# Optimization experiments

Hardware: AMD Instinct MI355X
Metric: run time of the kernel (lower is better)

## Reference

```python
import jax, jax.numpy as jnp
import numpy as np

B, N, C, H = 4, 2048, 1024, 16
D = C // H  # head_dim


def setup_inputs() -> dict:
    key = jax.random.key(0)
    ks = jax.random.split(key, 9)
    s = 1.0 / np.sqrt(C)
    return {
        "x": jax.random.normal(ks[0], (B, N, C), dtype=jnp.float32),
        "Wq": jax.random.uniform(ks[1], (C, C), jnp.float32, -s, s),
        "bq": jax.random.uniform(ks[2], (C,), jnp.float32, -s, s),
        "Wk": jax.random.uniform(ks[3], (C, C), jnp.float32, -s, s),
        "bk": jax.random.uniform(ks[4], (C,), jnp.float32, -s, s),
        "Wv": jax.random.uniform(ks[5], (C, C), jnp.float32, -s, s),
        "bv": jax.random.uniform(ks[6], (C,), jnp.float32, -s, s),
        "Wo": jax.random.uniform(ks[7], (C, C), jnp.float32, -s, s),
        "bo": jax.random.uniform(ks[8], (C,), jnp.float32, -s, s),
    }


def reference(x, Wq, bq, Wk, bk, Wv, bv, Wo, bo):
    # QKV projections -> [B, H, N, D]
    def proj(W, b):
        y = jnp.einsum('bnc,cd->bnd', x, W) + b
        return y.reshape(B, N, H, D).transpose(0, 2, 1, 3)

    q = proj(Wq, bq)
    k = proj(Wk, bk)
    v = proj(Wv, bv)

    scale = 1.0 / np.sqrt(D).astype(np.float32)
    scores = jnp.einsum('bhnd,bhmd->bhnm', q, k) * scale  # [B,H,N,N]
    probs = jax.nn.softmax(scores, axis=-1)
    out = jnp.einsum('bhnm,bhmd->bhnd', probs, v)  # [B,H,N,D]
    out = out.transpose(0, 2, 1, 3).reshape(B, N, C)
    return jnp.einsum('bnc,cd->bnd', out, Wo) + bo
```

## Files before the change

### kernel.cpp

```cpp
#include <hip/hip_runtime.h>
#include <hip/hip_bf16.h>
#include <stdint.h>


#define DEV __device__ __forceinline__

typedef unsigned short u16;
typedef __attribute__((ext_vector_type(8))) _Float16 f16x8;
typedef __attribute__((ext_vector_type(2))) _Float16 f16x2;
typedef __attribute__((ext_vector_type(4))) float f32x4;

DEV u16 f2h(float f) {
    _Float16 h = (_Float16)f;
    return __builtin_bit_cast(u16, h);
}

DEV unsigned int pk2h(float a, float b) {
    return __builtin_bit_cast(unsigned int, __builtin_amdgcn_cvt_pkrtz(a, b));
}

#define GLD16(gp, lp)                                                         \
    __builtin_amdgcn_global_load_lds(                                         \
        (__attribute__((address_space(1))) void*)(gp),                        \
        (__attribute__((address_space(3))) void*)(lp), 16, 0, 0)

DEV f32x4 mfma16(f16x8 a, f16x8 b, f32x4 c) {
    return __builtin_amdgcn_mfma_f32_16x16x32_f16(a, b, c, 0, 0, 0);
}

__global__ void cast_fuse(const float* __restrict__ x,
                          const float* __restrict__ Wq, const float* __restrict__ Wk,
                          const float* __restrict__ Wv, const float* __restrict__ Wo,
                          u16* __restrict__ xb, u16* __restrict__ Wt4) {
    __shared__ float lds[64 * 68];
    int bid = blockIdx.x, tid = threadIdx.x;
    if (bid < 4096) {
        size_t base = (size_t)bid * 2048 + (size_t)tid * 8;
        float4 v0 = *(const float4*)(x + base);
        float4 v1 = *(const float4*)(x + base + 4);
        union { u16 u[8]; uint4 v; } p;
        p.u[0] = f2h(v0.x); p.u[1] = f2h(v0.y); p.u[2] = f2h(v0.z); p.u[3] = f2h(v0.w);
        p.u[4] = f2h(v1.x); p.u[5] = f2h(v1.y); p.u[6] = f2h(v1.z); p.u[7] = f2h(v1.w);
        *(uint4*)(xb + base) = p.v;
        return;
    }
    bid -= 4096;
    int wsel = bid >> 8, t = bid & 255;
    int k0 = (t >> 4) * 64, n0 = (t & 15) * 64;
    const float* W = wsel == 0 ? Wq : wsel == 1 ? Wk : wsel == 2 ? Wv : Wo;
    u16* Wt = Wt4 + (size_t)wsel * 1048576;
#pragma unroll
    for (int i = 0; i < 4; i++) {
        int slot = tid * 4 + i * 1024;
        int rr = slot >> 6, cc = slot & 63;
        float4 v = *(const float4*)(W + (size_t)(k0 + rr) * 1024 + n0 + cc);
        *(float4*)(&lds[rr * 68 + cc]) = v;
    }
    __syncthreads();
    int n = tid >> 2, kc = (tid & 3) * 16;
    union { u16 u[16]; uint4 v[2]; } p;
#pragma unroll
    for (int j = 0; j < 16; j++) p.u[j] = f2h(lds[(kc + j) * 68 + n]);
    u16* dst = Wt + (size_t)(n0 + n) * 1024 + k0 + kc;
    *(uint4*)(dst) = p.v[0];
    *(uint4*)(dst + 8) = p.v[1];
}

DEV void gemm_core(const u16* __restrict__ A, const u16* __restrict__ Wt,
                   int m0, int n0, f32x4 (&acc)[4][4]) {
    __shared__ u16 Alds[2][128 * 32];
    __shared__ u16 Blds[2][128 * 32];
    const int tid = threadIdx.x, lane = tid & 63;
    const int w = tid >> 6, g = lane >> 4, r16 = lane & 15;
    const int wm = (w >> 1) * 64, wn = (w & 1) * 64;
#pragma unroll
    for (int i = 0; i < 4; i++)
#pragma unroll
        for (int j = 0; j < 4; j++) acc[i][j] = f32x4{0.f, 0.f, 0.f, 0.f};

    auto stage = [&](int buf, int kt) {
        int k0 = kt * 64;
#pragma unroll
        for (int i = 0; i < 2; i++) {
            int slot = i * 4096 + tid * 16;
            int rr = slot >> 6, cc = slot & 63;
            GLD16((const char*)A + (size_t)(m0 + rr) * 2048 + k0 + cc,
                  (char*)Alds[buf] + slot);
            GLD16((const char*)Wt + (size_t)(n0 + rr) * 2048 + k0 + cc,
                  (char*)Blds[buf] + slot);
        }
    };
    stage(0, 0);
    __syncthreads();

    for (int kt = 0; kt < 32; ++kt) {
        int cur = kt & 1;
        if (kt < 31) stage(cur ^ 1, kt + 1);
        f16x8 af[4], bf[4];
#pragma unroll
        for (int i = 0; i < 4; i++) {
            af[i] = *(const f16x8*)((const char*)Alds[cur] + (wm + i * 16 + r16) * 64 + g * 16);
            bf[i] = *(const f16x8*)((const char*)Blds[cur] + (wn + i * 16 + r16) * 64 + g * 16);
        }
#pragma unroll
        for (int i = 0; i < 4; i++)
#pragma unroll
            for (int j = 0; j < 4; j++) acc[i][j] = mfma16(af[i], bf[j], acc[i][j]);
        __syncthreads();
    }
}

__global__ __launch_bounds__(256, 2) void gemm_qkv(
    const u16* __restrict__ xb, const u16* __restrict__ Wt4,
    const float* __restrict__ bq, const float* __restrict__ bk,
    const float* __restrict__ bv,
    u16* __restrict__ Qo, u16* __restrict__ Ko, u16* __restrict__ Vo) {
    int m0 = blockIdx.x * 128, n0 = blockIdx.y * 128, z = blockIdx.z;
    const u16* Wt = Wt4 + (size_t)z * 1048576;
    const float* bias = z == 0 ? bq : z == 1 ? bk : bv;
    u16* Out = z == 0 ? Qo : z == 1 ? Ko : Vo;
    const float sc = (z == 0) ? 0.125f * 1.44269504f : 1.0f;
    f32x4 acc[4][4];
    gemm_core(xb, Wt, m0, n0, acc);
    const int lane = threadIdx.x & 63, w = threadIdx.x >> 6;
    const int g = lane >> 4, r16 = lane & 15;
    const int wm = (w >> 1) * 64, wn = (w & 1) * 64;
#pragma unroll
    for (int j = 0; j < 4; j++) {
        int c = n0 + wn + j * 16 + r16;
        float bb = bias[c];
        int h = c >> 6, d = c & 63;
#pragma unroll
        for (int i = 0; i < 4; i++) {
#pragma unroll
            for (int rr = 0; rr < 4; rr++) {
                int m = m0 + wm + i * 16 + g * 4 + rr;
                int b = m >> 11, n = m & 2047;
                Out[(((size_t)(b * 16 + h)) * 2048 + n) * 64 + d] =
                    f2h((acc[i][j][rr] + bb) * sc);
            }
        }
    }
}

__global__ __launch_bounds__(256, 2) void gemm_out(
    const u16* __restrict__ AO, const u16* __restrict__ Wt,
    const float* __restrict__ bo, float* __restrict__ Out) {
    int m0 = blockIdx.x * 128, n0 = blockIdx.y * 128;
    f32x4 acc[4][4];
    gemm_core(AO, Wt, m0, n0, acc);
    const int lane = threadIdx.x & 63, w = threadIdx.x >> 6;
    const int g = lane >> 4, r16 = lane & 15;
    const int wm = (w >> 1) * 64, wn = (w & 1) * 64;
#pragma unroll
    for (int j = 0; j < 4; j++) {
        int c = n0 + wn + j * 16 + r16;
        float bb = bo[c];
#pragma unroll
        for (int i = 0; i < 4; i++) {
#pragma unroll
            for (int rr = 0; rr < 4; rr++) {
                int m = m0 + wm + i * 16 + g * 4 + rr;
                Out[(size_t)m * 1024 + c] = acc[i][j][rr] + bb;
            }
        }
    }
}

__global__ void transpose_v(const u16* __restrict__ V, u16* __restrict__ VT) {
    __shared__ u16 lds[64 * 66];
    int bh = blockIdx.x >> 5, n0 = (blockIdx.x & 31) * 64;
    const u16* Vb = V + (size_t)bh * 2048 * 64;
    u16* VTb = VT + (size_t)bh * 64 * 2048;
    int tid = threadIdx.x;
#pragma unroll
    for (int i = 0; i < 8; i++) {
        int p = tid + i * 256;
        int rr = p >> 5, c2 = (p & 31) * 2;
        unsigned int val = *(const unsigned int*)(Vb + (size_t)(n0 + rr) * 64 + c2);
        *(unsigned int*)(&lds[rr * 66 + c2]) = val;
    }
    __syncthreads();
#pragma unroll
    for (int i = 0; i < 2; i++) {
        int s = tid * 8 + i * 2048;
        int d = s >> 6, ns = s & 63;
        union { u16 u[8]; uint4 v; } p;
#pragma unroll
        for (int j = 0; j < 8; j++) p.u[j] = lds[(ns + j) * 66 + d];
        *(uint4*)(VTb + (size_t)d * 2048 + n0 + ns) = p.v;
    }
}

__global__ __launch_bounds__(256, 2) void attn_k(
    const u16* __restrict__ Q, const u16* __restrict__ K,
    const u16* __restrict__ VT, u16* __restrict__ AO) {
    __shared__ char Klds[2][16384];
    __shared__ char Vlds[2][16384];
    __shared__ char Plds[4][4096];
    const int bh = blockIdx.x, q0 = blockIdx.y * 128;
    const int tid = threadIdx.x, lane = tid & 63, w = tid >> 6;
    const int g = lane >> 4, r16 = lane & 15;
    const char* Qb = (const char*)(Q + (size_t)bh * 2048 * 64);
    const char* Kb = (const char*)(K + (size_t)bh * 2048 * 64);
    const char* VTb = (const char*)(VT + (size_t)bh * 64 * 2048);
    char* Pw = Plds[w];
    const f32x4 ZZ = {0.f, 0.f, 0.f, 0.f};

    f16x8 qf[2][2];
#pragma unroll
    for (int qg = 0; qg < 2; qg++)
#pragma unroll
        for (int ks = 0; ks < 2; ks++)
            qf[qg][ks] = *(const f16x8*)(Qb + (size_t)(q0 + w * 32 + qg * 16 + r16) * 128 +
                                         ks * 64 + g * 16);
    f16x8 onesf;
#pragma unroll
    for (int j = 0; j < 8; j++) onesf[j] = (_Float16)1.0f;

    f32x4 oacc[2][4], lacc[2];
#pragma unroll
    for (int qg = 0; qg < 2; qg++) {
#pragma unroll
        for (int dg = 0; dg < 4; dg++) oacc[qg][dg] = ZZ;
        lacc[qg] = ZZ;
    }

    auto stage = [&](int buf, int t) {
#pragma unroll
        for (int i = 0; i < 4; i++) {
            int slot = i * 4096 + tid * 16;
            {
                int rr = slot >> 7, cc = slot & 127;
                GLD16(Kb + (size_t)(t * 128 + rr) * 128 + (cc ^ ((rr & 7) << 4)),
                      Klds[buf] + slot);
            }
            {
                int rr = slot >> 8, cc = slot & 255;
                GLD16(VTb + (size_t)rr * 4096 + t * 256 + (cc ^ ((rr & 7) << 4)),
                      Vlds[buf] + slot);
            }
        }
    };
    stage(0, 0);
    __syncthreads();

    for (int t = 0; t < 16; ++t) {
        const int cur = t & 1;
        if (t < 15) stage(cur ^ 1, t + 1);
        const char* Kl = Klds[cur];
        const char* Vl = Vlds[cur];

        f32x4 sacc[8][2];
        __builtin_amdgcn_s_setprio(1);
#pragma unroll
        for (int kg = 0; kg < 8; kg++) {
            int row = kg * 16 + r16, sw = (row & 7) << 4;
            f16x8 kf0 = *(const f16x8*)(Kl + row * 128 + ((g * 16) ^ sw));
            f16x8 kf1 = *(const f16x8*)(Kl + row * 128 + ((64 + g * 16) ^ sw));
#pragma unroll
            for (int qg = 0; qg < 2; qg++) {
                sacc[kg][qg] = mfma16(kf0, qf[qg][0], ZZ);
                sacc[kg][qg] = mfma16(kf1, qf[qg][1], sacc[kg][qg]);
            }
        }
        __builtin_amdgcn_s_setprio(0);

#pragma unroll
        for (int h = 0; h < 2; h++) {
#pragma unroll
            for (int qg = 0; qg < 2; qg++) {
#pragma unroll
                for (int kg2 = 0; kg2 < 4; kg2++) {
                    int kg = h * 4 + kg2;
                    uint2 pk;
                    pk.x = pk2h(exp2f(sacc[kg][qg][0]), exp2f(sacc[kg][qg][1]));
                    pk.y = pk2h(exp2f(sacc[kg][qg][2]), exp2f(sacc[kg][qg][3]));
                    *(uint2*)(Pw + (qg * 16 + r16) * 128 +
                              ((kg2 * 32 + g * 8) ^ ((r16 & 7) << 4))) = pk;
                }
            }
            __builtin_amdgcn_s_setprio(1);
#pragma unroll
            for (int ks2 = 0; ks2 < 2; ks2++) {
                f16x8 pf[2], vf[4];
#pragma unroll
                for (int qg = 0; qg < 2; qg++) {
                    int row = qg * 16 + r16;
                    pf[qg] = *(const f16x8*)(Pw + row * 128 +
                                             ((ks2 * 64 + g * 16) ^ ((r16 & 7) << 4)));
                }
#pragma unroll
                for (int dg = 0; dg < 4; dg++) {
                    int row = dg * 16 + r16;
                    vf[dg] = *(const f16x8*)(Vl + row * 256 +
                                             ((h * 128 + ks2 * 64 + g * 16) ^ ((row & 7) << 4)));
                }
#pragma unroll
                for (int qg = 0; qg < 2; qg++) {
#pragma unroll
                    for (int dg = 0; dg < 4; dg++)
                        oacc[qg][dg] = mfma16(pf[qg], vf[dg], oacc[qg][dg]);
                    lacc[qg] = mfma16(pf[qg], onesf, lacc[qg]);
                }
            }
            __builtin_amdgcn_s_setprio(0);
        }
        __syncthreads();
    }

    const int b = bh >> 4, h = bh & 15;
#pragma unroll
    for (int qg = 0; qg < 2; qg++) {
        float li[4];
#pragma unroll
        for (int rr = 0; rr < 4; rr++) li[rr] = 1.0f / lacc[qg][rr];
#pragma unroll
        for (int dg = 0; dg < 4; dg++) {
            int d = dg * 16 + r16;
#pragma unroll
            for (int rr = 0; rr < 4; rr++) {
                int nrow = q0 + w * 32 + qg * 16 + g * 4 + rr;
                AO[((size_t)(b * 2048 + nrow)) * 1024 + h * 64 + d] =
                    f2h(oacc[qg][dg][rr] * li[rr]);
            }
        }
    }
}

extern "C" void kernel_launch(void* const* d_in, const int* in_sizes, int n_in,
                              void* d_out, int out_size, void* d_ws, size_t ws_size,
                              hipStream_t stream) {
    const float* x = (const float*)d_in[0];
    const float* Wq = (const float*)d_in[1];
    const float* bq = (const float*)d_in[2];
    const float* Wk = (const float*)d_in[3];
    const float* bk = (const float*)d_in[4];
    const float* Wv = (const float*)d_in[5];
    const float* bv = (const float*)d_in[6];
    const float* Wo = (const float*)d_in[7];
    const float* bo = (const float*)d_in[8];

    char* ws = (char*)d_ws;
    u16* xb  = (u16*)(ws);
    u16* Wt  = (u16*)(ws + (16ull << 20));
    u16* Qb  = (u16*)(ws + (24ull << 20));
    u16* Kb  = (u16*)(ws + (40ull << 20));
    u16* Vb  = (u16*)(ws + (56ull << 20));
    u16* VTb = (u16*)(ws + (72ull << 20));
    u16* AO  = (u16*)(ws + (88ull << 20));

    cast_fuse<<<dim3(5120), dim3(256), 0, stream>>>(x, Wq, Wk, Wv, Wo, xb, Wt);
    gemm_qkv<<<dim3(64, 8, 3), dim3(256), 0, stream>>>(xb, Wt, bq, bk, bv, Qb, Kb, Vb);
    transpose_v<<<dim3(2048), dim3(256), 0, stream>>>(Vb, VTb);
    attn_k<<<dim3(64, 16), dim3(256), 0, stream>>>(Qb, Kb, VTb, AO);
    gemm_out<<<dim3(64, 8), dim3(256), 0, stream>>>(AO, Wt + 3ull * 1048576, bo,
                                                    (float*)d_out);
}
```

Baseline: 311.3 us.

## Enlarge GEMM tiles to 256x256 with swizzled LDS and interleaved pipeline

Replaces the 128x128, 4-wave GEMM core with a 256x256, 8-wave core for the QKV and output projections. It uses K-steps of 128, an XOR swizzle on the LDS layout to cut bank conflicts, and staged half-tile loads interleaved with MFMA phases under s_setprio and explicit barriers. The intent is to raise arithmetic intensity and hide global-to-LDS latency behind compute. The cost is far fewer blocks (384 and 128, versus a CU count of 256 on MI355X), so the wave fills the GPU poorly. The design also carries heavy LDS usage (128KB per block), register pressure, and many barriers.

Measured after the change: 340.4 us. 1.09x slower.

```diff
diff --git a/kernel.cpp b/kernel.cpp
--- a/kernel.cpp
+++ b/kernel.cpp
@@ -7,7 +7,6 @@
 
 typedef unsigned short u16;
 typedef __attribute__((ext_vector_type(8))) _Float16 f16x8;
-typedef __attribute__((ext_vector_type(2))) _Float16 f16x2;
 typedef __attribute__((ext_vector_type(4))) float f32x4;
 
 DEV u16 f2h(float f) {
@@ -27,6 +26,8 @@
 DEV f32x4 mfma16(f16x8 a, f16x8 b, f32x4 c) {
     return __builtin_amdgcn_mfma_f32_16x16x32_f16(a, b, c, 0, 0, 0);
 }
+
+DEV int swz(int lin) { return lin ^ (((lin >> 9) & 1) << 5); }
 
 __global__ void cast_fuse(const float* __restrict__ x,
                           const float* __restrict__ Wq, const float* __restrict__ Wk,
@@ -66,102 +67,152 @@
     *(uint4*)(dst + 8) = p.v[1];
 }
 
-DEV void gemm_core(const u16* __restrict__ A, const u16* __restrict__ Wt,
-                   int m0, int n0, f32x4 (&acc)[4][4]) {
-    __shared__ u16 Alds[2][128 * 32];
-    __shared__ u16 Blds[2][128 * 32];
+DEV void gemm_core256(const u16* __restrict__ A, const u16* __restrict__ Bw,
+                      int m0, int n0, f32x4 (&acc)[8][4]) {
+    __shared__ u16 Al[2][2][128 * 64];
+    __shared__ u16 Bl[2][2][128 * 64];
     const int tid = threadIdx.x, lane = tid & 63;
     const int w = tid >> 6, g = lane >> 4, r16 = lane & 15;
-    const int wm = (w >> 1) * 64, wn = (w & 1) * 64;
-#pragma unroll
-    for (int i = 0; i < 4; i++)
-#pragma unroll
-        for (int j = 0; j < 4; j++) acc[i][j] = f32x4{0.f, 0.f, 0.f, 0.f};
-
-    auto stage = [&](int buf, int kt) {
-        int k0 = kt * 64;
-#pragma unroll
-        for (int i = 0; i < 2; i++) {
-            int slot = i * 4096 + tid * 16;
-            int rr = slot >> 6, cc = slot & 63;
-            GLD16((const char*)A + (size_t)(m0 + rr) * 2048 + k0 + cc,
-                  (char*)Alds[buf] + slot);
-            GLD16((const char*)Wt + (size_t)(n0 + rr) * 2048 + k0 + cc,
-                  (char*)Blds[buf] + slot);
+    const int wm_id = w >> 2, wnh = (w & 3) >> 1, wnl = w & 1;
+
+#pragma unroll
+    for (int mi = 0; mi < 8; mi++)
+#pragma unroll
+        for (int nj = 0; nj < 4; nj++) acc[mi][nj] = f32x4{0.f, 0.f, 0.f, 0.f};
+
+    auto stage = [&](int buf, int h, int T) {
+        const bool isB = (h & 2) != 0;
+        const int half = h & 1;
+        char* dst = (char*)(isB ? Bl[buf][half] : Al[buf][half]);
+        const char* src = (const char*)(isB ? Bw : A);
+        const int r0 = (isB ? n0 : m0) + half * 128;
+#pragma unroll
+        for (int j = 0; j < 2; ++j) {
+            int slot = j * 8192 + tid * 16;
+            int lin = swz(slot);
+            int row = lin >> 7, c2 = lin & 127;
+            GLD16(src + (size_t)(r0 + row) * 2048 + T * 128 + c2, dst + slot);
         }
     };
-    stage(0, 0);
-    __syncthreads();
-
-    for (int kt = 0; kt < 32; ++kt) {
-        int cur = kt & 1;
-        if (kt < 31) stage(cur ^ 1, kt + 1);
-        f16x8 af[4], bf[4];
-#pragma unroll
-        for (int i = 0; i < 4; i++) {
-            af[i] = *(const f16x8*)((const char*)Alds[cur] + (wm + i * 16 + r16) * 64 + g * 16);
-            bf[i] = *(const f16x8*)((const char*)Blds[cur] + (wn + i * 16 + r16) * 64 + g * 16);
-        }
-#pragma unroll
-        for (int i = 0; i < 4; i++)
-#pragma unroll
-            for (int j = 0; j < 4; j++) acc[i][j] = mfma16(af[i], bf[j], acc[i][j]);
-        __syncthreads();
-    }
-}
-
-__global__ __launch_bounds__(256, 2) void gemm_qkv(
+    auto lda = [&](f16x8 (&af)[4][2], int mq, const char* Ah) {
+#pragma unroll
+        for (int mi = 0; mi < 4; ++mi)
+#pragma unroll
+            for (int ks = 0; ks < 2; ++ks) {
+                int lin = (mq * 64 + mi * 16 + r16) * 128 + ks * 64 + g * 16;
+                af[mi][ks] = *(const f16x8*)(Ah + swz(lin));
+            }
+    };
+    auto ldb = [&](f16x8 (&bf)[2][2], int nq, const char* Bh) {
+#pragma unroll
+        for (int nj = 0; nj < 2; ++nj)
+#pragma unroll
+            for (int ks = 0; ks < 2; ++ks) {
+                int lin = (wnl * 64 + nq * 32 + nj * 16 + r16) * 128 + ks * 64 + g * 16;
+                bf[nj][ks] = *(const f16x8*)(Bh + swz(lin));
+            }
+    };
+    auto mm = [&](int mq, int nq, f16x8 (&af)[4][2], f16x8 (&bf)[2][2]) {
+        __builtin_amdgcn_s_setprio(1);
+#pragma unroll
+        for (int mi = 0; mi < 4; ++mi)
+#pragma unroll
+            for (int nj = 0; nj < 2; ++nj) {
+                f32x4 c = acc[mq * 4 + mi][nq * 2 + nj];
+                c = mfma16(af[mi][0], bf[nj][0], c);
+                c = mfma16(af[mi][1], bf[nj][1], c);
+                acc[mq * 4 + mi][nq * 2 + nj] = c;
+            }
+        __builtin_amdgcn_s_setprio(0);
+    };
+
+#pragma unroll
+    for (int h = 0; h < 4; ++h) stage(0, h, 0);
+    stage(1, 0, 1);
+    asm volatile("s_waitcnt vmcnt(2)" ::: "memory");
+    __builtin_amdgcn_s_barrier();
+
+    for (int T = 0; T < 16; ++T) {
+        const int buf = T & 1;
+        const char* Ah = (const char*)Al[buf][wm_id];
+        const char* Bh = (const char*)Bl[buf][wnh];
+        f16x8 af[4][2], bfA[2][2], bfB[2][2];
+        lda(af, 0, Ah);
+        ldb(bfA, 0, Bh);
+        if (T + 1 < 16) stage(buf ^ 1, 1, T + 1);
+        __builtin_amdgcn_s_barrier();
+        mm(0, 0, af, bfA);
+        __builtin_amdgcn_s_barrier();
+        ldb(bfB, 1, Bh);
+        if (T + 1 < 16) stage(buf ^ 1, 2, T + 1);
+        __builtin_amdgcn_s_barrier();
+        mm(0, 1, af, bfB);
+        __builtin_amdgcn_s_barrier();
+        lda(af, 1, Ah);
+        if (T + 1 < 16) stage(buf ^ 1, 3, T + 1);
+        __builtin_amdgcn_s_barrier();
+        mm(1, 0, af, bfA);
+        __builtin_amdgcn_s_barrier();
+        if (T + 2 < 16) stage(buf, 0, T + 2);
+        __builtin_amdgcn_s_barrier();
+        mm(1, 1, af, bfB);
+        asm volatile("s_waitcnt vmcnt(2)" ::: "memory");
+        __builtin_amdgcn_s_barrier();
+    }
+}
+
+__global__ __launch_bounds__(512, 2) void gemm_qkv(
     const u16* __restrict__ xb, const u16* __restrict__ Wt4,
     const float* __restrict__ bq, const float* __restrict__ bk,
     const float* __restrict__ bv,
     u16* __restrict__ Qo, u16* __restrict__ Ko, u16* __restrict__ Vo) {
-    int m0 = blockIdx.x * 128, n0 = blockIdx.y * 128, z = blockIdx.z;
+    int m0 = blockIdx.x * 256, n0 = blockIdx.y * 256, z = blockIdx.z;
     const u16* Wt = Wt4 + (size_t)z * 1048576;
     const float* bias = z == 0 ? bq : z == 1 ? bk : bv;
     u16* Out = z == 0 ? Qo : z == 1 ? Ko : Vo;
     const float sc = (z == 0) ? 0.125f * 1.44269504f : 1.0f;
-    f32x4 acc[4][4];
-    gemm_core(xb, Wt, m0, n0, acc);
+    f32x4 acc[8][4];
+    gemm_core256(xb, Wt, m0, n0, acc);
     const int lane = threadIdx.x & 63, w = threadIdx.x >> 6;
     const int g = lane >> 4, r16 = lane & 15;
-    const int wm = (w >> 1) * 64, wn = (w & 1) * 64;
-#pragma unroll
-    for (int j = 0; j < 4; j++) {
-        int c = n0 + wn + j * 16 + r16;
+    const int wm0 = m0 + (w >> 2) * 128, wn0 = n0 + (w & 3) * 64;
+#pragma unroll
+    for (int nj = 0; nj < 4; nj++) {
+        int c = wn0 + nj * 16 + r16;
         float bb = bias[c];
         int h = c >> 6, d = c & 63;
 #pragma unroll
-        for (int i = 0; i < 4; i++) {
+        for (int mi = 0; mi < 8; mi++) {
 #pragma unroll
             for (int rr = 0; rr < 4; rr++) {
-                int m = m0 + wm + i * 16 + g * 4 + rr;
+                int m = wm0 + mi * 16 + g * 4 + rr;
                 int b = m >> 11, n = m & 2047;
                 Out[(((size_t)(b * 16 + h)) * 2048 + n) * 64 + d] =
-                    f2h((acc[i][j][rr] + bb) * sc);
-            }
-        }
-    }
-}
-
-__global__ __launch_bounds__(256, 2) void gemm_out(
+                    f2h((acc[mi][nj][rr] + bb) * sc);
+            }
+        }
+    }
+}
+
+__global__ __launch_bounds__(512, 2) void gemm_out(
     const u16* __restrict__ AO, const u16* __restrict__ Wt,
     const float* __restrict__ bo, float* __restrict__ Out) {
-    int m0 = blockIdx.x * 128, n0 = blockIdx.y * 128;
-    f32x4 acc[4][4];
-    gemm_core(AO, Wt, m0, n0, acc);
+    int m0 = blockIdx.x * 256, n0 = blockIdx.y * 256;
+    f32x4 acc[8][4];
+    gemm_core256(AO, Wt, m0, n0, acc);
     const int lane = threadIdx.x & 63, w = threadIdx.x >> 6;
     const int g = lane >> 4, r16 = lane & 15;
-    const int wm = (w >> 1) * 64, wn = (w & 1) * 64;
-#pragma unroll
-    for (int j = 0; j < 4; j++) {
-        int c = n0 + wn + j * 16 + r16;
+    const int wm0 = m0 + (w >> 2) * 128, wn0 = n0 + (w & 3) * 64;
+#pragma unroll
+    for (int nj = 0; nj < 4; nj++) {
+        int c = wn0 + nj * 16 + r16;
         float bb = bo[c];
 #pragma unroll
-        for (int i = 0; i < 4; i++) {
+        for (int mi = 0; mi < 8; mi++) {
 #pragma unroll
             for (int rr = 0; rr < 4; rr++) {
-                int m = m0 + wm + i * 16 + g * 4 + rr;
-                Out[(size_t)m * 1024 + c] = acc[i][j][rr] + bb;
+                int m = wm0 + mi * 16 + g * 4 + rr;
+                Out[(size_t)m * 1024 + c] = acc[mi][nj][rr] + bb;
             }
         }
     }
@@ -351,9 +402,9 @@
     u16* AO  = (u16*)(ws + (88ull << 20));
 
     cast_fuse<<<dim3(5120), dim3(256), 0, stream>>>(x, Wq, Wk, Wv, Wo, xb, Wt);
-    gemm_qkv<<<dim3(64, 8, 3), dim3(256), 0, stream>>>(xb, Wt, bq, bk, bv, Qb, Kb, Vb);
+    gemm_qkv<<<dim3(32, 4, 3), dim3(512), 0, stream>>>(xb, Wt, bq, bk, bv, Qb, Kb, Vb);
     transpose_v<<<dim3(2048), dim3(256), 0, stream>>>(Vb, VTb);
     attn_k<<<dim3(64, 16), dim3(256), 0, stream>>>(Qb, Kb, VTb, AO);
-    gemm_out<<<dim3(64, 8), dim3(256), 0, stream>>>(AO, Wt + 3ull * 1048576, bo,
+    gemm_out<<<dim3(32, 4), dim3(512), 0, stream>>>(AO, Wt + 3ull * 1048576, bo,
                                                     (float*)d_out);
 }
```

## Use 8 waves per attention block and stage QKV epilogue through LDS

Applied to the files above, without the earlier changes.

The attention kernel now runs 512 threads per block with 8 waves, each owning 16 query rows instead of 32. This halves per-wave accumulator registers and spreads the K/V tile staging across more threads, in exchange for more K/V LDS reads per query row and one block per CU's worth of LDS. Separately, the QKV GEMM epilogue writes its tile into LDS and then emits coalesced 16-byte stores into the head-major layout, replacing scattered 2-byte stores. The extra LDS buffer and barrier in the GEMM may reduce its occupancy.

New measurement: 314.3 us. Within noise of the previous version (+1.0%).

```diff
diff --git a/kernel.cpp b/kernel.cpp
--- a/kernel.cpp
+++ b/kernel.cpp
@@ -7,7 +7,6 @@
 
 typedef unsigned short u16;
 typedef __attribute__((ext_vector_type(8))) _Float16 f16x8;
-typedef __attribute__((ext_vector_type(2))) _Float16 f16x2;
 typedef __attribute__((ext_vector_type(4))) float f32x4;
 
 DEV u16 f2h(float f) {
@@ -122,23 +121,35 @@
     const float sc = (z == 0) ? 0.125f * 1.44269504f : 1.0f;
     f32x4 acc[4][4];
     gemm_core(xb, Wt, m0, n0, acc);
-    const int lane = threadIdx.x & 63, w = threadIdx.x >> 6;
+
+    __shared__ u16 Clds[128 * 136];
+    const int tid = threadIdx.x, lane = tid & 63, w = tid >> 6;
     const int g = lane >> 4, r16 = lane & 15;
     const int wm = (w >> 1) * 64, wn = (w & 1) * 64;
 #pragma unroll
     for (int j = 0; j < 4; j++) {
-        int c = n0 + wn + j * 16 + r16;
-        float bb = bias[c];
-        int h = c >> 6, d = c & 63;
-#pragma unroll
-        for (int i = 0; i < 4; i++) {
+        int nl = wn + j * 16 + r16;
+        float bb = bias[n0 + nl];
+#pragma unroll
+        for (int i = 0; i < 4; i++)
 #pragma unroll
             for (int rr = 0; rr < 4; rr++) {
-                int m = m0 + wm + i * 16 + g * 4 + rr;
-                int b = m >> 11, n = m & 2047;
-                Out[(((size_t)(b * 16 + h)) * 2048 + n) * 64 + d] =
-                    f2h((acc[i][j][rr] + bb) * sc);
-            }
+                int ml = wm + i * 16 + g * 4 + rr;
+                Clds[ml * 136 + nl] = f2h((acc[i][j][rr] + bb) * sc);
+            }
+    }
+    __syncthreads();
+    const int b = m0 >> 11, nst = m0 & 2047;
+#pragma unroll
+    for (int s = 0; s < 2; s++) {
+        int h = (n0 + s * 64) >> 6;
+        u16* obase = Out + (((size_t)(b * 16 + h)) * 2048 + nst) * 64;
+#pragma unroll
+        for (int p = 0; p < 4; p++) {
+            int idx = p * 256 + tid;
+            int r = idx >> 3, c8 = (idx & 7) * 8;
+            uint4 v = *(const uint4*)(&Clds[r * 136 + s * 64 + c8]);
+            *(uint4*)(obase + (size_t)r * 64 + c8) = v;
         }
     }
 }
@@ -192,12 +203,12 @@
     }
 }
 
-__global__ __launch_bounds__(256, 2) void attn_k(
+__global__ __launch_bounds__(512, 4) void attn_k(
     const u16* __restrict__ Q, const u16* __restrict__ K,
     const u16* __restrict__ VT, u16* __restrict__ AO) {
     __shared__ char Klds[2][16384];
     __shared__ char Vlds[2][16384];
-    __shared__ char Plds[4][4096];
+    __shared__ char Plds[8][2048];
     const int bh = blockIdx.x, q0 = blockIdx.y * 128;
     const int tid = threadIdx.x, lane = tid & 63, w = tid >> 6;
     const int g = lane >> 4, r16 = lane & 15;
@@ -207,29 +218,24 @@
     char* Pw = Plds[w];
     const f32x4 ZZ = {0.f, 0.f, 0.f, 0.f};
 
-    f16x8 qf[2][2];
-#pragma unroll
-    for (int qg = 0; qg < 2; qg++)
-#pragma unroll
-        for (int ks = 0; ks < 2; ks++)
-            qf[qg][ks] = *(const f16x8*)(Qb + (size_t)(q0 + w * 32 + qg * 16 + r16) * 128 +
-                                         ks * 64 + g * 16);
+    f16x8 qf[2];
+#pragma unroll
+    for (int ks = 0; ks < 2; ks++)
+        qf[ks] = *(const f16x8*)(Qb + (size_t)(q0 + w * 16 + r16) * 128 +
+                                 ks * 64 + g * 16);
     f16x8 onesf;
 #pragma unroll
     for (int j = 0; j < 8; j++) onesf[j] = (_Float16)1.0f;
 
-    f32x4 oacc[2][4], lacc[2];
-#pragma unroll
-    for (int qg = 0; qg < 2; qg++) {
-#pragma unroll
-        for (int dg = 0; dg < 4; dg++) oacc[qg][dg] = ZZ;
-        lacc[qg] = ZZ;
-    }
+    f32x4 oacc[4], lacc;
+#pragma unroll
+    for (int dg = 0; dg < 4; dg++) oacc[dg] = ZZ;
+    lacc = ZZ;
 
     auto stage = [&](int buf, int t) {
 #pragma unroll
-        for (int i = 0; i < 4; i++) {
-            int slot = i * 4096 + tid * 16;
+        for (int i = 0; i < 2; i++) {
+            int slot = i * 8192 + tid * 16;
             {
                 int rr = slot >> 7, cc = slot & 127;
                 GLD16(Kb + (size_t)(t * 128 + rr) * 128 + (cc ^ ((rr & 7) << 4)),
@@ -251,45 +257,35 @@
         const char* Kl = Klds[cur];
         const char* Vl = Vlds[cur];
 
-        f32x4 sacc[8][2];
+        f32x4 sacc[8];
         __builtin_amdgcn_s_setprio(1);
 #pragma unroll
         for (int kg = 0; kg < 8; kg++) {
             int row = kg * 16 + r16, sw = (row & 7) << 4;
             f16x8 kf0 = *(const f16x8*)(Kl + row * 128 + ((g * 16) ^ sw));
             f16x8 kf1 = *(const f16x8*)(Kl + row * 128 + ((64 + g * 16) ^ sw));
-#pragma unroll
-            for (int qg = 0; qg < 2; qg++) {
-                sacc[kg][qg] = mfma16(kf0, qf[qg][0], ZZ);
-                sacc[kg][qg] = mfma16(kf1, qf[qg][1], sacc[kg][qg]);
-            }
+            sacc[kg] = mfma16(kf0, qf[0], ZZ);
+            sacc[kg] = mfma16(kf1, qf[1], sacc[kg]);
         }
         __builtin_amdgcn_s_setprio(0);
 
 #pragma unroll
         for (int h = 0; h < 2; h++) {
 #pragma unroll
-            for (int qg = 0; qg < 2; qg++) {
-#pragma unroll
-                for (int kg2 = 0; kg2 < 4; kg2++) {
-                    int kg = h * 4 + kg2;
-                    uint2 pk;
-                    pk.x = pk2h(exp2f(sacc[kg][qg][0]), exp2f(sacc[kg][qg][1]));
-                    pk.y = pk2h(exp2f(sacc[kg][qg][2]), exp2f(sacc[kg][qg][3]));
-                    *(uint2*)(Pw + (qg * 16 + r16) * 128 +
-                              ((kg2 * 32 + g * 8) ^ ((r16 & 7) << 4))) = pk;
-                }
+            for (int kg2 = 0; kg2 < 4; kg2++) {
+                int kg = h * 4 + kg2;
+                uint2 pk;
+                pk.x = pk2h(exp2f(sacc[kg][0]), exp2f(sacc[kg][1]));
+                pk.y = pk2h(exp2f(sacc[kg][2]), exp2f(sacc[kg][3]));
+                *(uint2*)(Pw + r16 * 128 +
+                          ((kg2 * 32 + g * 8) ^ ((r16 & 7) << 4))) = pk;
             }
             __builtin_amdgcn_s_setprio(1);
 #pragma unroll
             for (int ks2 = 0; ks2 < 2; ks2++) {
-                f16x8 pf[2], vf[4];
-#pragma unroll
-                for (int qg = 0; qg < 2; qg++) {
-                    int row = qg * 16 + r16;
-                    pf[qg] = *(const f16x8*)(Pw + row * 128 +
-                                             ((ks2 * 64 + g * 16) ^ ((r16 & 7) << 4)));
-                }
+                f16x8 pf = *(const f16x8*)(Pw + r16 * 128 +
+                                           ((ks2 * 64 + g * 16) ^ ((r16 & 7) << 4)));
+                f16x8 vf[4];
 #pragma unroll
                 for (int dg = 0; dg < 4; dg++) {
                     int row = dg * 16 + r16;
@@ -297,12 +293,9 @@
                                              ((h * 128 + ks2 * 64 + g * 16) ^ ((row & 7) << 4)));
                 }
 #pragma unroll
-                for (int qg = 0; qg < 2; qg++) {
-#pragma unroll
-                    for (int dg = 0; dg < 4; dg++)
-                        oacc[qg][dg] = mfma16(pf[qg], vf[dg], oacc[qg][dg]);
-                    lacc[qg] = mfma16(pf[qg], onesf, lacc[qg]);
-                }
+                for (int dg = 0; dg < 4; dg++)
+                    oacc[dg] = mfma16(pf, vf[dg], oacc[dg]);
+                lacc = mfma16(pf, onesf, lacc);
             }
             __builtin_amdgcn_s_setprio(0);
         }
@@ -310,20 +303,17 @@
     }
 
     const int b = bh >> 4, h = bh & 15;
-#pragma unroll
-    for (int qg = 0; qg < 2; qg++) {
-        float li[4];
-#pragma unroll
-        for (int rr = 0; rr < 4; rr++) li[rr] = 1.0f / lacc[qg][rr];
-#pragma unroll
-        for (int dg = 0; dg < 4; dg++) {
-            int d = dg * 16 + r16;
-#pragma unroll
-            for (int rr = 0; rr < 4; rr++) {
-                int nrow = q0 + w * 32 + qg * 16 + g * 4 + rr;
-                AO[((size_t)(b * 2048 + nrow)) * 1024 + h * 64 + d] =
-                    f2h(oacc[qg][dg][rr] * li[rr]);
-            }
+    float li[4];
+#pragma unroll
+    for (int rr = 0; rr < 4; rr++) li[rr] = 1.0f / lacc[rr];
+#pragma unroll
+    for (int dg = 0; dg < 4; dg++) {
+        int d = dg * 16 + r16;
+#pragma unroll
+        for (int rr = 0; rr < 4; rr++) {
+            int nrow = q0 + w * 16 + g * 4 + rr;
+            AO[((size_t)(b * 2048 + nrow)) * 1024 + h * 64 + d] =
+                f2h(oacc[dg][rr] * li[rr]);
         }
     }
 }
@@ -353,7 +343,7 @@
     cast_fuse<<<dim3(5120), dim3(256), 0, stream>>>(x, Wq, Wk, Wv, Wo, xb, Wt);
     gemm_qkv<<<dim3(64, 8, 3), dim3(256), 0, stream>>>(xb, Wt, bq, bk, bv, Qb, Kb, Vb);
     transpose_v<<<dim3(2048), dim3(256), 0, stream>>>(Vb, VTb);
-    attn_k<<<dim3(64, 16), dim3(256), 0, stream>>>(Qb, Kb, VTb, AO);
+    attn_k<<<dim3(64, 16), dim3(512), 0, stream>>>(Qb, Kb, VTb, AO);
     gemm_out<<<dim3(64, 8), dim3(256), 0, stream>>>(AO, Wt + 3ull * 1048576, bo,
                                                     (float*)d_out);
 }
```
